# Performance work log

Measured on AMD Instinct MI355X. Metric: run time of the kernel, lower is better.

The kernel has to match this reference:

```python
import jax, jax.numpy as jnp
import numpy as np

SOS_TOKEN = 0
VOCAB, EMBED, HIDDEN = 32000, 256, 256


def setup_inputs() -> dict:
    key = jax.random.key(0)
    ks = jax.random.split(key, 10)
    B, S, T = 32, 128, 128
    s = 0.05
    return {
        "encoder_outputs": jax.random.normal(ks[0], (B, S, HIDDEN), jnp.float32),
        "encoder_hidden": jax.random.normal(ks[1], (1, B, HIDDEN), jnp.float32),
        "target_tensor": jax.random.randint(ks[2], (B, T), 0, VOCAB),
        "embedding": jax.random.normal(ks[3], (VOCAB, EMBED), jnp.float32) * s,
        "W_ih": jax.random.normal(ks[4], (3 * HIDDEN, EMBED + HIDDEN), jnp.float32) * s,
        "W_hh": jax.random.normal(ks[5], (3 * HIDDEN, HIDDEN), jnp.float32) * s,
        "b_ih": jax.random.normal(ks[6], (3 * HIDDEN,), jnp.float32) * s,
        "b_hh": jax.random.normal(ks[7], (3 * HIDDEN,), jnp.float32) * s,
        "W_out": jax.random.normal(ks[8], (VOCAB, HIDDEN), jnp.float32) * s,
        "b_out": jax.random.normal(ks[9], (VOCAB,), jnp.float32) * s,
    }


def _decode(encoder_outputs, encoder_hidden, target_tensor, embedding,
            W_ih, W_hh, b_ih, b_hh, W_out, b_out):
    B, T = target_tensor.shape
    # full teacher forcing: decoder input at step t is target[t-1], step 0 is SOS
    dec_in = jnp.concatenate(
        [jnp.full((B, 1), SOS_TOKEN, dtype=target_tensor.dtype), target_tensor[:, :-1]], axis=1)
    emb = embedding[dec_in]                                     # (B,T,E)
    # attention: query = embedded input, key = value = encoder_outputs
    scores = jnp.einsum("bte,bse->bts", emb, encoder_outputs)   # (B,T,S)
    attn = jax.nn.softmax(scores, axis=2)
    context = jnp.einsum("bts,bsh->bth", attn, encoder_outputs)  # (B,T,H)
    x_seq = jnp.concatenate([emb, context], axis=2)             # (B,T,E+H)
    x_seq = jnp.swapaxes(x_seq, 0, 1)                           # (T,B,E+H)

    def gru_step(h, x):
        gi = x @ W_ih.T + b_ih                                  # (B,3H)
        gh = h @ W_hh.T + b_hh
        i_r, i_z, i_n = jnp.split(gi, 3, axis=1)
        h_r, h_z, h_n = jnp.split(gh, 3, axis=1)
        r = jax.nn.sigmoid(i_r + h_r)
        z = jax.nn.sigmoid(i_z + h_z)
        n = jnp.tanh(i_n + r * h_n)
        h_new = (1.0 - z) * n + z * h
        return h_new, h_new

    h0 = encoder_hidden[0]                                      # (B,H)
    _, hs = jax.lax.scan(gru_step, h0, x_seq)                   # (T,B,H)
    logits = hs @ W_out.T + b_out                               # (T,B,V)
    return jnp.swapaxes(logits, 0, 1)                           # (B,T,V)


def reference(encoder_outputs, encoder_hidden, target_tensor, embedding,
              W_ih, W_hh, b_ih, b_hh, W_out, b_out):
    return _decode(encoder_outputs, encoder_hidden, target_tensor, embedding,
                   W_ih, W_hh, b_ih, b_hh, W_out, b_out)
```

## Files before the change

### kernel.cpp

```cpp
#include <hip/hip_runtime.h>
#include <hip/hip_bf16.h>
#include <stdint.h>

typedef float    f32x4  __attribute__((ext_vector_type(4)));
typedef __bf16   bf16x8 __attribute__((ext_vector_type(8)));
typedef _Float16 f16x8  __attribute__((ext_vector_type(8)));
typedef _Float16 h2v    __attribute__((ext_vector_type(2)));

#define B_ 32
#define S_ 128
#define T_ 128
#define H_ 256
#define E_ 256
#define V_ 32000

__device__ __forceinline__ void gll16(const void* g, void* l) {
  __builtin_amdgcn_global_load_lds(
      (const __attribute__((address_space(1))) uint32_t*)g,
      (__attribute__((address_space(3))) uint32_t*)l,
      16, 0, 0);
}

__device__ __forceinline__ uint32_t pack_pair(float a, float b) {
  unsigned short lo = __builtin_bit_cast(unsigned short, (_Float16)a);
  unsigned short hi = __builtin_bit_cast(unsigned short, (_Float16)b);
  return (uint32_t)lo | ((uint32_t)hi << 16);
}

__device__ __forceinline__ uint32_t pack_bf16(float a, float b) {
  return (uint32_t)__builtin_bit_cast(unsigned short, __float2bfloat16(a)) |
         ((uint32_t)__builtin_bit_cast(unsigned short, __float2bfloat16(b)) << 16);
}

__device__ __forceinline__ float dot2(uint32_t w, uint32_t h, float acc) {
#if __has_builtin(__builtin_amdgcn_fdot2)
  return __builtin_amdgcn_fdot2(__builtin_bit_cast(h2v, w),
                                __builtin_bit_cast(h2v, h), acc, false);
#else
  h2v wv = __builtin_bit_cast(h2v, w);
  h2v hv = __builtin_bit_cast(h2v, h);
  return acc + (float)wv.x * (float)hv.x + (float)wv.y * (float)hv.y;
#endif
}

__device__ __forceinline__ float sigmoid_fast(float x) {
  return __fdividef(1.f, 1.f + __expf(-x));
}
__device__ __forceinline__ float tanh_fast(float x) {
  float e = __expf(2.f * fabsf(x));
  float t = 1.f - __fdividef(2.f, e + 1.f);
  return copysignf(t, x);
}

__global__ __launch_bounds__(256) void cvt_bf16_kernel(
    const float* __restrict__ src, uint32_t* __restrict__ dst, int n) {
  int i = (blockIdx.x * 256 + threadIdx.x) * 8;
  if (i + 7 < n) {
    float4 a = *(const float4*)(src + i);
    float4 b = *(const float4*)(src + i + 4);
    uint4 o;
    o.x = pack_bf16(a.x, a.y);
    o.y = pack_bf16(a.z, a.w);
    o.z = pack_bf16(b.x, b.y);
    o.w = pack_bf16(b.z, b.w);
    *(uint4*)(dst + (i >> 1)) = o;
  }
}

__global__ __launch_bounds__(256) void cvt_f16_kernel(
    const float* __restrict__ src, uint32_t* __restrict__ dst, int n) {
  int i = (blockIdx.x * 256 + threadIdx.x) * 4;
  if (i + 3 < n) {
    float4 v = *(const float4*)(src + i);
    uint2 p;
    p.x = pack_pair(v.x, v.y);
    p.y = pack_pair(v.z, v.w);
    *(uint2*)(dst + (i >> 1)) = p;
  }
}

__global__ __launch_bounds__(256) void pack_whh(
    const float* __restrict__ Whh, uint32_t* __restrict__ Wp) {
  __shared__ float lds[32][257];
  int j0 = blockIdx.x * 32;
  int tid = threadIdx.x;
  #pragma unroll 4
  for (int i = 0; i < 32; ++i)
    lds[i][tid] = Whh[(size_t)(j0 + i) * 256 + tid];
  __syncthreads();
  #pragma unroll 4
  for (int i = 0; i < 16; ++i) {
    int e = i * 256 + tid;
    int k2 = e >> 5;
    int jj = e & 31;
    Wp[(size_t)k2 * 768 + j0 + jj] = pack_pair(lds[jj][2 * k2], lds[jj][2 * k2 + 1]);
  }
}

__global__ __launch_bounds__(256) void attn_kernel(
    const float* __restrict__ enc,
    const int*   __restrict__ tgt,
    const float* __restrict__ embt,
    uint32_t*    __restrict__ xh)
{
  int b   = blockIdx.x;
  int tc  = blockIdx.y;
  int tid = threadIdx.x;
  __shared__ __align__(16) float e_sh[256];
  __shared__ float attn_sh[128];
  __shared__ float red_sh[4];
  const float* encb = enc + (size_t)b * S_ * H_;

  for (int tt = 0; tt < 8; ++tt) {
    int t = tc * 8 + tt;
    int tok = (t == 0) ? 0 : tgt[b * T_ + t - 1];
    float ev = embt[(size_t)tok * E_ + tid];
    e_sh[tid] = ev;
    {
      float other = __shfl_xor(ev, 1);
      if (!(tid & 1))
        xh[(size_t)(t * B_ + b) * 256 + (tid >> 1)] = pack_pair(ev, other);
    }
    __syncthreads();

    float sc = 0.f;
    if (tid < 128) {
      const float* er = encb + tid * H_;
      #pragma unroll 8
      for (int k = 0; k < 256; k += 4) {
        float4 e4 = *(const float4*)(e_sh + k);
        float4 r4 = *(const float4*)(er + k);
        sc += e4.x * r4.x; sc += e4.y * r4.y; sc += e4.z * r4.z; sc += e4.w * r4.w;
      }
      float mx = sc;
      #pragma unroll
      for (int o = 32; o > 0; o >>= 1) mx = fmaxf(mx, __shfl_xor(mx, o, 64));
      if ((tid & 63) == 0) red_sh[tid >> 6] = mx;
    }
    __syncthreads();
    float gmax = fmaxf(red_sh[0], red_sh[1]);
    float p = 0.f;
    if (tid < 128) {
      p = __expf(sc - gmax);
      float s = p;
      #pragma unroll
      for (int o = 32; o > 0; o >>= 1) s += __shfl_xor(s, o, 64);
      if ((tid & 63) == 0) red_sh[2 + (tid >> 6)] = s;
    }
    __syncthreads();
    float tot = red_sh[2] + red_sh[3];
    if (tid < 128) attn_sh[tid] = p / tot;
    __syncthreads();

    float ctx = 0.f;
    #pragma unroll 4
    for (int s = 0; s < 128; ++s) ctx += attn_sh[s] * encb[s * H_ + tid];
    {
      float other = __shfl_xor(ctx, 1);
      if (!(tid & 1))
        xh[(size_t)(t * B_ + b) * 256 + 128 + (tid >> 1)] = pack_pair(ctx, other);
    }
    __syncthreads();
  }
}

__global__ __launch_bounds__(256) void gi_gemm_f16(
    const _Float16* __restrict__ A,
    const _Float16* __restrict__ Bm,
    const float* __restrict__ bih,
    float* __restrict__ gi)
{
  __shared__ _Float16 sA[128 * 64];
  __shared__ _Float16 sB[128 * 64];
  int tid = threadIdx.x;
  int n0 = blockIdx.x * 128;
  int m0 = blockIdx.y * 128;
  int lane = tid & 63;
  int wave = tid >> 6;
  int wm = (wave >> 1) * 64;
  int wn = (wave & 1) * 64;
  int srow = tid >> 3;
  int sk   = (tid & 7) * 8;
  f32x4 acc[4][4] = {};

  for (int kt = 0; kt < 512; kt += 64) {
    #pragma unroll
    for (int it = 0; it < 4; ++it) {
      int row = it * 32 + srow;
      gll16(A  + (size_t)(m0 + row) * 512 + kt + sk, &sA[row * 64 + sk]);
      gll16(Bm + (size_t)(n0 + row) * 512 + kt + sk, &sB[row * 64 + sk]);
    }
    __syncthreads();
    #pragma unroll
    for (int kk = 0; kk < 2; ++kk) {
      f16x8 af[4], bfr[4];
      #pragma unroll
      for (int m = 0; m < 4; ++m)
        af[m] = *(const f16x8*)&sA[(wm + m * 16 + (lane & 15)) * 64 + kk * 32 + (lane >> 4) * 8];
      #pragma unroll
      for (int n = 0; n < 4; ++n)
        bfr[n] = *(const f16x8*)&sB[(wn + n * 16 + (lane & 15)) * 64 + kk * 32 + (lane >> 4) * 8];
      #pragma unroll
      for (int m = 0; m < 4; ++m)
        #pragma unroll
        for (int n = 0; n < 4; ++n)
          acc[m][n] = __builtin_amdgcn_mfma_f32_16x16x32_f16(af[m], bfr[n], acc[m][n], 0, 0, 0);
    }
    __syncthreads();
  }

  #pragma unroll
  for (int n = 0; n < 4; ++n) {
    int col = n0 + wn + n * 16 + (lane & 15);
    float bv = bih[col];
    #pragma unroll
    for (int m = 0; m < 4; ++m) {
      int rbase = m0 + wm + m * 16 + (lane >> 4) * 4;
      #pragma unroll
      for (int r = 0; r < 4; ++r)
        gi[(size_t)(rbase + r) * 768 + col] = acc[m][n][r] + bv;
    }
  }
}

__global__ __launch_bounds__(768) void gru_kernel(
    const float*    __restrict__ gi,
    const uint32_t* __restrict__ Wp,
    const float*    __restrict__ bhh,
    const float*    __restrict__ h0,
    __hip_bfloat16* __restrict__ hs)
{
  int b   = blockIdx.x;
  int tid = threadIdx.x;
  int role = tid >> 8;
  int j    = tid & 255;
  __shared__ __align__(16) uint32_t h2[128];
  __shared__ float r_sh[256];
  __shared__ float z_sh[256];

  uint32_t w[128];
  #pragma unroll
  for (int i = 0; i < 128; ++i) w[i] = Wp[(size_t)i * 768 + tid];
  float bj = bhh[tid];

  float hprev = 0.f;
  if (role == 2) {
    hprev = h0[b * 256 + j];
    float other = __shfl_xor(hprev, 1);
    if (!(j & 1)) h2[j >> 1] = pack_pair(hprev, other);
  }
  float gval = gi[(size_t)b * 768 + tid];
  __syncthreads();

  for (int t = 0; t < 128; ++t) {
    float gnext = 0.f;
    if (t < 127) gnext = gi[(size_t)((t + 1) * 32 + b) * 768 + tid];

    float a0 = 0.f, a1 = 0.f, a2 = 0.f, a3 = 0.f;
    float a4 = 0.f, a5 = 0.f, a6 = 0.f, a7 = 0.f;
    #pragma unroll
    for (int k8 = 0; k8 < 16; ++k8) {
      uint4 ha = *(const uint4*)&h2[k8 * 8];
      uint4 hb = *(const uint4*)&h2[k8 * 8 + 4];
      a0 = dot2(w[k8 * 8 + 0], ha.x, a0);
      a1 = dot2(w[k8 * 8 + 1], ha.y, a1);
      a2 = dot2(w[k8 * 8 + 2], ha.z, a2);
      a3 = dot2(w[k8 * 8 + 3], ha.w, a3);
      a4 = dot2(w[k8 * 8 + 4], hb.x, a4);
      a5 = dot2(w[k8 * 8 + 5], hb.y, a5);
      a6 = dot2(w[k8 * 8 + 6], hb.z, a6);
      a7 = dot2(w[k8 * 8 + 7], hb.w, a7);
    }
    float gh = ((a0 + a1) + (a2 + a3)) + ((a4 + a5) + (a6 + a7)) + bj;

    if (role == 0)      r_sh[j] = sigmoid_fast(gval + gh);
    else if (role == 1) z_sh[j] = sigmoid_fast(gval + gh);
    __syncthreads();

    if (role == 2) {
      float r = r_sh[j];
      float z = z_sh[j];
      float n = tanh_fast(gval + r * gh);
      float hn = (1.f - z) * n + z * hprev;
      hprev = hn;
      hs[(size_t)(t * 32 + b) * 256 + j] = __float2bfloat16(hn);
      float other = __shfl_xor(hn, 1);
      if (!(j & 1)) h2[j >> 1] = pack_pair(hn, other);
    }
    gval = gnext;
    __syncthreads();
  }
}

__global__ __launch_bounds__(256) void logits_gemm(
    const __hip_bfloat16* __restrict__ A,
    const __hip_bfloat16* __restrict__ Bm,
    const float* __restrict__ bout,
    float* __restrict__ out)
{
  __shared__ __hip_bfloat16 sA[128 * 64];
  __shared__ __hip_bfloat16 sB[128 * 64];
  int tid = threadIdx.x;
  int bid = blockIdx.x;
  int chunk = bid & 7;
  int local = bid >> 3;
  int m0 = (chunk * 4 + (local & 3)) * 128;
  int n0 = (local >> 2) * 128;
  int lane = tid & 63;
  int wave = tid >> 6;
  int wm = (wave >> 1) * 64;
  int wn = (wave & 1) * 64;
  int srow = tid >> 3;
  int schunk = tid & 7;
  f32x4 acc[4][4] = {};

  for (int kt = 0; kt < 256; kt += 64) {
    #pragma unroll
    for (int it = 0; it < 4; ++it) {
      int row = it * 32 + srow;
      int gc = ((schunk ^ (row & 7)) * 8);
      gll16(A  + (size_t)(m0 + row) * 256 + kt + gc, &sA[row * 64 + schunk * 8]);
      gll16(Bm + (size_t)(n0 + row) * 256 + kt + gc, &sB[row * 64 + schunk * 8]);
    }
    __syncthreads();
    #pragma unroll
    for (int kk = 0; kk < 2; ++kk) {
      bf16x8 af[4], bfr[4];
      #pragma unroll
      for (int m = 0; m < 4; ++m) {
        int r = wm + m * 16 + (lane & 15);
        int pc = ((kk * 4 + (lane >> 4)) ^ (r & 7)) * 8;
        af[m] = *(const bf16x8*)&sA[r * 64 + pc];
      }
      #pragma unroll
      for (int n = 0; n < 4; ++n) {
        int r = wn + n * 16 + (lane & 15);
        int pc = ((kk * 4 + (lane >> 4)) ^ (r & 7)) * 8;
        bfr[n] = *(const bf16x8*)&sB[r * 64 + pc];
      }
      #pragma unroll
      for (int m = 0; m < 4; ++m)
        #pragma unroll
        for (int n = 0; n < 4; ++n)
          acc[m][n] = __builtin_amdgcn_mfma_f32_16x16x32_bf16(bfr[n], af[m], acc[m][n], 0, 0, 0);
    }
    __syncthreads();
  }

  #pragma unroll
  for (int m = 0; m < 4; ++m) {
    int row = m0 + wm + m * 16 + (lane & 15);
    int t  = row >> 5;
    int bb = row & 31;
    float* orow = out + (size_t)(bb * 128 + t) * 32000;
    #pragma unroll
    for (int n = 0; n < 4; ++n) {
      int col0 = n0 + wn + n * 16 + (lane >> 4) * 4;
      f32x4 bv = *(const f32x4*)&bout[col0];
      *(f32x4*)&orow[col0] = acc[m][n] + bv;
    }
  }
}

extern "C" void kernel_launch(void* const* d_in, const int* in_sizes, int n_in,
                              void* d_out, int out_size, void* d_ws, size_t ws_size,
                              hipStream_t stream) {
  const float* enc  = (const float*)d_in[0];
  const float* ench = (const float*)d_in[1];
  const int*   tgt  = (const int*)d_in[2];
  const float* embt = (const float*)d_in[3];
  const float* Wih  = (const float*)d_in[4];
  const float* Whh  = (const float*)d_in[5];
  const float* bih  = (const float*)d_in[6];
  const float* bhh  = (const float*)d_in[7];
  const float* Wout = (const float*)d_in[8];
  const float* bout = (const float*)d_in[9];
  float* out = (float*)d_out;

  char* ws = (char*)d_ws;
  float*          gi    = (float*)(ws);
  __hip_bfloat16* hs    = (__hip_bfloat16*)(ws + 12582912);
  __hip_bfloat16* woutb = (__hip_bfloat16*)(ws + 14680064);
  uint32_t*       xh    = (uint32_t*)(ws + 31064064);
  uint32_t*       wihh  = (uint32_t*)(ws + 35258368);

  uint32_t* Wp = (uint32_t*)(out + ((size_t)out_size - 98304));

  cvt_bf16_kernel<<<4000, 256, 0, stream>>>(Wout, (uint32_t*)woutb, V_ * H_);
  cvt_f16_kernel<<<384, 256, 0, stream>>>(Wih, wihh, 768 * 512);
  pack_whh<<<24, 256, 0, stream>>>(Whh, Wp);
  attn_kernel<<<dim3(32, 16), 256, 0, stream>>>(enc, tgt, embt, xh);
  gi_gemm_f16<<<dim3(6, 32), 256, 0, stream>>>((const _Float16*)xh, (const _Float16*)wihh, bih, gi);
  gru_kernel<<<32, 768, 0, stream>>>(gi, Wp, bhh, ench, hs);
  logits_gemm<<<8000, 256, 0, stream>>>(hs, woutb, bout, out);
}
```

Baseline: 488.3 us.

## Drop LDS staging in logits GEMM, load MFMA fragments directly from global

The logits GEMM no longer stages A and B tiles through shared memory with barriers. Each wave now owns 32 rows and all 128 columns of the block tile. It keeps its full A fragments (all of K=256) in registers and streams B fragments straight from global/L2 into the MFMAs. This removes LDS traffic and __syncthreads, but every wave re-reads the full B tile from cache and register pressure rises.

```diff
diff --git a/kernel.cpp b/kernel.cpp
--- a/kernel.cpp
+++ b/kernel.cpp
@@ -298,8 +298,6 @@
     const float* __restrict__ bout,
     float* __restrict__ out)
 {
-  __shared__ __hip_bfloat16 sA[128 * 64];
-  __shared__ __hip_bfloat16 sB[128 * 64];
   int tid = threadIdx.x;
   int bid = blockIdx.x;
   int chunk = bid & 7;
@@ -308,54 +306,39 @@
   int n0 = (local >> 2) * 128;
   int lane = tid & 63;
   int wave = tid >> 6;
-  int wm = (wave >> 1) * 64;
-  int wn = (wave & 1) * 64;
-  int srow = tid >> 3;
-  int schunk = tid & 7;
-  f32x4 acc[4][4] = {};
-
-  for (int kt = 0; kt < 256; kt += 64) {
-    #pragma unroll
-    for (int it = 0; it < 4; ++it) {
-      int row = it * 32 + srow;
-      int gc = ((schunk ^ (row & 7)) * 8);
-      gll16(A  + (size_t)(m0 + row) * 256 + kt + gc, &sA[row * 64 + schunk * 8]);
-      gll16(Bm + (size_t)(n0 + row) * 256 + kt + gc, &sB[row * 64 + schunk * 8]);
-    }
-    __syncthreads();
-    #pragma unroll
-    for (int kk = 0; kk < 2; ++kk) {
-      bf16x8 af[4], bfr[4];
-      #pragma unroll
-      for (int m = 0; m < 4; ++m) {
-        int r = wm + m * 16 + (lane & 15);
-        int pc = ((kk * 4 + (lane >> 4)) ^ (r & 7)) * 8;
-        af[m] = *(const bf16x8*)&sA[r * 64 + pc];
-      }
-      #pragma unroll
-      for (int n = 0; n < 4; ++n) {
-        int r = wn + n * 16 + (lane & 15);
-        int pc = ((kk * 4 + (lane >> 4)) ^ (r & 7)) * 8;
-        bfr[n] = *(const bf16x8*)&sB[r * 64 + pc];
-      }
-      #pragma unroll
-      for (int m = 0; m < 4; ++m)
-        #pragma unroll
-        for (int n = 0; n < 4; ++n)
-          acc[m][n] = __builtin_amdgcn_mfma_f32_16x16x32_bf16(bfr[n], af[m], acc[m][n], 0, 0, 0);
-    }
-    __syncthreads();
-  }
-
-  #pragma unroll
-  for (int m = 0; m < 4; ++m) {
-    int row = m0 + wm + m * 16 + (lane & 15);
+  int rbase = m0 + wave * 32;
+  int lr = lane & 15;
+  int lk = (lane >> 4) * 8;
+
+  bf16x8 af[2][8];
+  #pragma unroll
+  for (int m = 0; m < 2; ++m)
+    #pragma unroll
+    for (int k8 = 0; k8 < 8; ++k8)
+      af[m][k8] = *(const bf16x8*)&A[(size_t)(rbase + m * 16 + lr) * 256 + k8 * 32 + lk];
+
+  f32x4 acc[2][8] = {};
+
+  #pragma unroll
+  for (int k8 = 0; k8 < 8; ++k8) {
+    #pragma unroll
+    for (int n = 0; n < 8; ++n) {
+      bf16x8 bfr = *(const bf16x8*)&Bm[(size_t)(n0 + n * 16 + lr) * 256 + k8 * 32 + lk];
+      #pragma unroll
+      for (int m = 0; m < 2; ++m)
+        acc[m][n] = __builtin_amdgcn_mfma_f32_16x16x32_bf16(bfr, af[m][k8], acc[m][n], 0, 0, 0);
+    }
+  }
+
+  #pragma unroll
+  for (int m = 0; m < 2; ++m) {
+    int row = rbase + m * 16 + lr;
     int t  = row >> 5;
     int bb = row & 31;
     float* orow = out + (size_t)(bb * 128 + t) * 32000;
     #pragma unroll
-    for (int n = 0; n < 4; ++n) {
-      int col0 = n0 + wn + n * 16 + (lane >> 4) * 4;
+    for (int n = 0; n < 8; ++n) {
+      int col0 = n0 + n * 16 + (lane >> 4) * 4;
       f32x4 bv = *(const f32x4*)&bout[col0];
       *(f32x4*)&orow[col0] = acc[m][n] + bv;
     }
```

Measured after the change: 658.4 us. 34.8% more time.
